# Kernel optimization log

Measured on AMD Instinct MI355X. Metric: run time of the kernel, lower is better.

Reference implementation:

```python
import jax, jax.numpy as jnp
import numpy as np

HEADS = 8
DIM_HEAD = 64
SCALE = DIM_HEAD ** -0.5


def setup_inputs() -> dict:
    key = jax.random.key(0)
    ks = jax.random.split(key, 6)
    B, T, C, H, W = 16, 64, 512, 64, 64
    inner = HEADS * DIM_HEAD  # 512
    return {
        "vision_feature": jax.random.normal(ks[0], (B, C, H, W), jnp.float32),
        "language_feature": jax.random.normal(ks[1], (B, T, C), jnp.float32),
        "mask": jnp.ones((B, T), jnp.int32),  # unused by the module's forward
        "Wq": jax.random.normal(ks[2], (inner, C), jnp.float32) * (C ** -0.5),
        "Wk": jax.random.normal(ks[3], (inner, C), jnp.float32) * (C ** -0.5),
        "Wv": jax.random.normal(ks[4], (inner, C), jnp.float32) * (C ** -0.5),
        "Wo": jax.random.normal(ks[5], (C, inner), jnp.float32) * (inner ** -0.5),
    }


def reference(vision_feature, language_feature, mask, Wq, Wk, Wv, Wo):
    B, T, C = language_feature.shape
    _, _, H, W = vision_feature.shape
    S = H * W
    # 1x1 conv projections == matmuls over the channel dim
    q = jnp.einsum('btc,ic->bti', language_feature, Wq)           # (B, T, inner)
    vis = vision_feature.reshape(B, C, S)                          # (B, C, S)
    k = jnp.einsum('ic,bcs->bis', Wk, vis)                         # (B, inner, S)
    v = jnp.einsum('ic,bcs->bis', Wv, vis)                         # (B, inner, S)
    # split heads: channel index = n*dim_head + d  (n outermost)
    q = q.reshape(B, T, HEADS, DIM_HEAD).transpose(2, 0, 1, 3)     # (h, B, T, d)
    k = k.reshape(B, HEADS, DIM_HEAD, S).transpose(1, 0, 2, 3)     # (h, B, d, S)
    v = v.reshape(B, HEADS, DIM_HEAD, S).transpose(1, 0, 3, 2)     # (h, B, S, d)
    att = jax.nn.softmax(jnp.einsum('hbtd,hbds->hbts', q, k) * SCALE, axis=-1)
    out = jnp.einsum('hbts,hbsd->hbtd', att, v)                    # (h, B, T, d)
    # merge heads back: b (n c) tokens -> equivalently (B, T, h*d)
    out = out.transpose(1, 2, 0, 3).reshape(B, T, HEADS * DIM_HEAD)
    out = jnp.einsum('bti,oi->bto', out, Wo)                       # (B, T, C)
    return out
```

## Files before the change

### kernel.cpp

```cpp
#include <hip/hip_runtime.h>
#include <stdint.h>

typedef __attribute__((ext_vector_type(8))) short short8;
typedef __attribute__((ext_vector_type(4))) short short4v;
typedef __attribute__((ext_vector_type(4))) float float4v;
typedef __attribute__((ext_vector_type(8))) __bf16 bf16x8;

#define NCH 8

__device__ __forceinline__ float4v mfma16x16x32(short8 a, short8 b, float4v c) {
  return __builtin_amdgcn_mfma_f32_16x16x32_bf16(
      __builtin_bit_cast(bf16x8, a), __builtin_bit_cast(bf16x8, b), c, 0, 0, 0);
}

__device__ __forceinline__ short f2bf(float f) {
  uint32_t u = __builtin_bit_cast(uint32_t, f);
  u += 0x7fffu + ((u >> 16) & 1u);
  return (short)(u >> 16);
}

__device__ __forceinline__ float bf2f(short s) {
  return __builtin_bit_cast(float, ((uint32_t)(uint16_t)s) << 16);
}

__device__ __forceinline__ void load_lds16(const short* g, short* l) {
  __builtin_amdgcn_global_load_lds(
      (const __attribute__((address_space(1))) void*)g,
      (__attribute__((address_space(3))) void*)l, 16, 0, 0);
}

__global__ __launch_bounds__(256) void convert5(
    const float* __restrict__ sl, short* __restrict__ dl,
    const float* __restrict__ s1, short* __restrict__ d1,
    const float* __restrict__ s2, short* __restrict__ d2,
    const float* __restrict__ s3, short* __restrict__ d3,
    const float* __restrict__ s4, short* __restrict__ d4) {
  const float* src; short* dst; int n4;
  switch (blockIdx.y) {
    case 0: src = sl; dst = dl; n4 = 131072; break;
    case 1: src = s1; dst = d1; n4 = 65536; break;
    case 2: src = s2; dst = d2; n4 = 65536; break;
    case 3: src = s3; dst = d3; n4 = 65536; break;
    default: src = s4; dst = d4; n4 = 65536; break;
  }
  const int stride = gridDim.x * blockDim.x;
  for (int i = blockIdx.x * blockDim.x + threadIdx.x; i < n4; i += stride) {
    float4v v = *(const float4v*)(src + (long)i * 4);
    short4v o;
#pragma unroll
    for (int r = 0; r < 4; r++) o[r] = f2bf(v[r]);
    *(short4v*)(dst + (long)i * 4) = o;
  }
}

template <int TRANS_STORE, int OUT_F32>
__global__ __launch_bounds__(256) void gemm_nt(
    const short* __restrict__ A, long sA,
    const short* __restrict__ B, long sB,
    void* __restrict__ C, long sC,
    int K, int ldc, float scale) {
  __shared__ alignas(16) short lA[128 * 32];
  __shared__ alignas(16) short lB[128 * 32];
  const int tid = threadIdx.x;
  const int lane = tid & 63, w = tid >> 6;
  const int quad = lane >> 4, l16 = lane & 15;
  const int wm = w >> 1, wn = w & 1;
  const long m0 = (long)blockIdx.y * 128, n0 = (long)blockIdx.x * 128;
  A += blockIdx.z * sA;
  B += blockIdx.z * sB;

  float4v acc[4][4];
#pragma unroll
  for (int i = 0; i < 4; i++)
#pragma unroll
    for (int j = 0; j < 4; j++) acc[i][j] = (float4v)0.0f;

  const int srow = tid >> 2;
  const int scol = (tid & 3) * 8;

  for (int kt = 0; kt < K; kt += 32) {
    load_lds16(&A[(m0 + srow) * K + kt + scol], &lA[tid * 8]);
    load_lds16(&A[(m0 + 64 + srow) * K + kt + scol], &lA[2048 + tid * 8]);
    load_lds16(&B[(n0 + srow) * K + kt + scol], &lB[tid * 8]);
    load_lds16(&B[(n0 + 64 + srow) * K + kt + scol], &lB[2048 + tid * 8]);
    __syncthreads();

    short8 af[4], bf[4];
#pragma unroll
    for (int t = 0; t < 4; t++) {
      af[t] = *(const short8*)&lA[(wm * 64 + t * 16 + l16) * 32 + quad * 8];
      bf[t] = *(const short8*)&lB[(wn * 64 + t * 16 + l16) * 32 + quad * 8];
    }
#pragma unroll
    for (int i = 0; i < 4; i++)
#pragma unroll
      for (int j = 0; j < 4; j++)
        acc[i][j] = mfma16x16x32(af[i], bf[j], acc[i][j]);
    __syncthreads();
  }

  const int cm = wm * 64 + quad * 4;
  const int cn = wn * 64 + l16;
  if (OUT_F32) {
    float* Cf = (float*)C + blockIdx.z * sC;
#pragma unroll
    for (int i = 0; i < 4; i++)
#pragma unroll
      for (int j = 0; j < 4; j++) {
        const long gn = n0 + cn + j * 16;
#pragma unroll
        for (int r = 0; r < 4; r++)
          Cf[(m0 + cm + i * 16 + r) * (long)ldc + gn] = acc[i][j][r] * scale;
      }
  } else if (TRANS_STORE) {
    short* Cs = (short*)C + blockIdx.z * sC;
#pragma unroll
    for (int i = 0; i < 4; i++)
#pragma unroll
      for (int j = 0; j < 4; j++) {
        const long gm = m0 + cm + i * 16;
        const long gn = n0 + cn + j * 16;
        short4v pk;
#pragma unroll
        for (int r = 0; r < 4; r++) pk[r] = f2bf(acc[i][j][r] * scale);
        *(short4v*)&Cs[gn * (long)ldc + gm] = pk;
      }
  } else {
    short* Cs = (short*)C + blockIdx.z * sC;
#pragma unroll
    for (int i = 0; i < 4; i++)
#pragma unroll
      for (int j = 0; j < 4; j++) {
        const long gn = n0 + cn + j * 16;
#pragma unroll
        for (int r = 0; r < 4; r++)
          Cs[(m0 + cm + i * 16 + r) * (long)ldc + gn] = f2bf(acc[i][j][r] * scale);
      }
  }
}

__global__ __launch_bounds__(256) void transpose_f2b(
    const float* __restrict__ vis, short* __restrict__ visT) {
  __shared__ alignas(16) short buf[64][68];
  const int tid = threadIdx.x;
  const long bz = blockIdx.z;
  const long s0 = (long)blockIdx.x * 64;
  const long c0 = (long)blockIdx.y * 64;
  const float* src = vis + bz * 512 * 4096;
  short* dst = visT + bz * 4096 * 512;
  const int tr = tid >> 4;
  const int tc4 = (tid & 15) * 4;
#pragma unroll
  for (int i = 0; i < 4; i++) {
    const int c = tr + i * 16;
    float4v val = *(const float4v*)&src[(c0 + c) * 4096 + s0 + tc4];
    buf[tc4 + 0][c] = f2bf(val[0]);
    buf[tc4 + 1][c] = f2bf(val[1]);
    buf[tc4 + 2][c] = f2bf(val[2]);
    buf[tc4 + 3][c] = f2bf(val[3]);
  }
  __syncthreads();
#pragma unroll
  for (int i = 0; i < 4; i++) {
    const int s = tr + i * 16;
    short4v val = *(const short4v*)&buf[s][tc4];
    *(short4v*)&dst[(s0 + s) * 512 + c0 + tc4] = val;
  }
}

__global__ __launch_bounds__(256) void attn_part(
    const short* __restrict__ q, const short* __restrict__ kws,
    const short* __restrict__ vws, float* __restrict__ Opart,
    float* __restrict__ lpart, int b0) {
  const int h = blockIdx.x;
  const int bz = blockIdx.y;
  const int ch = blockIdx.z;
  const int tid = threadIdx.x;
  const int lane = tid & 63, w = tid >> 6;
  const int quad = lane >> 4, l16 = lane & 15;

  __shared__ alignas(16) short lq[64 * 64];
  __shared__ alignas(16) short lk[128 * 64];
  __shared__ alignas(16) short lv[64 * 128];
  __shared__ alignas(16) short lp[64 * 128];
  __shared__ float lsum[64];

  const short* qb = q + ((long)(b0 + bz) * 64) * 512 + h * 64;
  const short* kb = kws + (long)bz * 4096 * 512 + h * 64;
  const short* vb = vws + (long)bz * 512 * 4096 + (long)h * 64 * 4096;

  if (tid < 64) lsum[tid] = 0.0f;
  load_lds16(&qb[(tid >> 3) * 512 + (tid & 7) * 8], &lq[tid * 8]);
  load_lds16(&qb[(32 + (tid >> 3)) * 512 + (tid & 7) * 8], &lq[2048 + tid * 8]);
  __syncthreads();

  short8 aq[4][2];
#pragma unroll
  for (int mt = 0; mt < 4; mt++)
#pragma unroll
    for (int ks = 0; ks < 2; ks++)
      aq[mt][ks] = *(const short8*)&lq[(mt * 16 + l16) * 64 + ks * 32 + quad * 8];

  float4v osc[4];
#pragma unroll
  for (int mt = 0; mt < 4; mt++) osc[mt] = (float4v)0.0f;
  float lrow[4][4] = {};

  const int send = ch * 512 + 512;
  for (int s0 = ch * 512; s0 < send; s0 += 128) {
#pragma unroll
    for (int it = 0; it < 4; it++) {
      const int li = tid + it * 256;
      load_lds16(&kb[(long)(s0 + (li >> 3)) * 512 + (li & 7) * 8], &lk[li * 8]);
    }
#pragma unroll
    for (int it = 0; it < 4; it++) {
      const int li = tid + it * 256;
      load_lds16(&vb[(long)(li >> 4) * 4096 + s0 + (li & 15) * 8], &lv[li * 8]);
    }
    __syncthreads();

    float4v sc[4][2];
#pragma unroll
    for (int mt = 0; mt < 4; mt++)
#pragma unroll
      for (int jn = 0; jn < 2; jn++) sc[mt][jn] = (float4v)0.0f;
#pragma unroll
    for (int ks = 0; ks < 2; ks++) {
      short8 bk[2];
#pragma unroll
      for (int jn = 0; jn < 2; jn++)
        bk[jn] = *(const short8*)&lk[((2 * w + jn) * 16 + l16) * 64 + ks * 32 + quad * 8];
#pragma unroll
      for (int mt = 0; mt < 4; mt++)
#pragma unroll
        for (int jn = 0; jn < 2; jn++)
          sc[mt][jn] = mfma16x16x32(aq[mt][ks], bk[jn], sc[mt][jn]);
    }

#pragma unroll
    for (int mt = 0; mt < 4; mt++)
#pragma unroll
      for (int jn = 0; jn < 2; jn++)
#pragma unroll
        for (int r = 0; r < 4; r++) {
          const float scv = fminf(fmaxf(sc[mt][jn][r], -80.0f), 30.0f);
          const short sp = f2bf(__expf(scv));
          lrow[mt][r] += bf2f(sp);
          lp[(mt * 16 + quad * 4 + r) * 128 + (2 * w + jn) * 16 + l16] = sp;
        }
    __syncthreads();

#pragma unroll
    for (int ks = 0; ks < 4; ks++) {
      const short8 bv = *(const short8*)&lv[(w * 16 + l16) * 128 + ks * 32 + quad * 8];
#pragma unroll
      for (int mt = 0; mt < 4; mt++) {
        const short8 ap = *(const short8*)&lp[(mt * 16 + l16) * 128 + ks * 32 + quad * 8];
        osc[mt] = mfma16x16x32(ap, bv, osc[mt]);
      }
    }
    __syncthreads();
  }

#pragma unroll
  for (int mt = 0; mt < 4; mt++)
#pragma unroll
    for (int r = 0; r < 4; r++) {
      float v = lrow[mt][r];
      v += __shfl_xor(v, 1);
      v += __shfl_xor(v, 2);
      v += __shfl_xor(v, 4);
      v += __shfl_xor(v, 8);
      if (l16 == 0) atomicAdd(&lsum[mt * 16 + quad * 4 + r], v);
    }
  __syncthreads();

  const long bh = bz * 8 + h;
  float* op = Opart + ((bh * NCH + ch) * 64) * 64 + w * 16 + l16;
#pragma unroll
  for (int mt = 0; mt < 4; mt++)
#pragma unroll
    for (int r = 0; r < 4; r++)
      op[(long)(mt * 16 + quad * 4 + r) * 64] = osc[mt][r];
  if (tid < 64) lpart[(bh * NCH + ch) * 64 + tid] = lsum[tid];
}

__global__ __launch_bounds__(256) void attn_combine(
    const float* __restrict__ Opart, const float* __restrict__ lpart,
    short* __restrict__ tmp, int b0, int nbh) {
  const int total = nbh * 4096;
  for (int idx = blockIdx.x * 256 + threadIdx.x; idx < total;
       idx += gridDim.x * 256) {
    const int bh = idx >> 12;
    const int td = idx & 4095;
    const int t = td >> 6, d = td & 63;
    float o = 0.0f, l = 0.0f;
#pragma unroll
    for (int c = 0; c < NCH; c++) {
      o += Opart[((long)bh * NCH + c) * 4096 + td];
      l += lpart[(bh * NCH + c) * 64 + t];
    }
    const int b = b0 + (bh >> 3), h = bh & 7;
    tmp[((long)b * 64 + t) * 512 + h * 64 + d] = f2bf(o / l);
  }
}

extern "C" void kernel_launch(void* const* d_in, const int* in_sizes, int n_in,
                              void* d_out, int out_size, void* d_ws, size_t ws_size,
                              hipStream_t stream) {
  (void)in_sizes; (void)n_in; (void)out_size;
  const float* vis = (const float*)d_in[0];
  const float* lang = (const float*)d_in[1];
  const float* Wq = (const float*)d_in[3];
  const float* Wk = (const float*)d_in[4];
  const float* Wv = (const float*)d_in[5];
  const float* Wo = (const float*)d_in[6];
  float* out = (float*)d_out;

  char* ws = (char*)d_ws;
  const size_t MB = 1 << 20;
  short* q_ws = (short*)(ws + 0 * MB);
  short* tmp_ws = (short*)(ws + 1 * MB);
  short* langb = (short*)(ws + 2 * MB);
  short* Wqb = (short*)(ws + 3 * MB);
  short* Wkb = (short*)(ws + 3 * MB + 512 * 1024);
  short* Wvb = (short*)(ws + 4 * MB);
  short* Wob = (short*)(ws + 4 * MB + 512 * 1024);
  char* grp = ws + 5 * MB;

  const long batch_elems = 4096l * 512;
  int g = 16;
  const int cands[5] = {1, 2, 4, 8, 16};
  for (int ci = 0; ci < 5; ci++) {
    const size_t need = 5 * MB + 3ull * (16 / cands[ci]) * batch_elems * 2;
    if (need <= ws_size) { g = cands[ci]; break; }
  }
  const int Bg = 16 / g;
  short* visT = (short*)grp;
  short* k_ws = visT + (long)Bg * batch_elems;
  short* v_ws = k_ws + (long)Bg * batch_elems;
  float* Opart = (float*)visT;
  float* lptr = Opart + (long)Bg * 262144;

  convert5<<<dim3(128, 5), 256, 0, stream>>>(lang, langb, Wq, Wqb, Wk, Wkb,
                                             Wv, Wvb, Wo, Wob);

  gemm_nt<0, 0><<<dim3(4, 8, 1), 256, 0, stream>>>(langb, 0, Wqb, 0, q_ws, 0, 512, 512, 0.125f);

  for (int gi = 0; gi < g; gi++) {
    const int b0 = gi * Bg;
    transpose_f2b<<<dim3(64, 8, Bg), 256, 0, stream>>>(vis + (long)b0 * batch_elems, visT);
    gemm_nt<1, 0><<<dim3(32, 4, Bg), 256, 0, stream>>>(Wkb, 0, visT, batch_elems, k_ws, batch_elems, 512, 512, 1.0f);
    gemm_nt<0, 0><<<dim3(32, 4, Bg), 256, 0, stream>>>(Wvb, 0, visT, batch_elems, v_ws, batch_elems, 512, 4096, 1.0f);
    attn_part<<<dim3(8, Bg, NCH), 256, 0, stream>>>(q_ws, k_ws, v_ws, Opart, lptr, b0);
    attn_combine<<<512, 256, 0, stream>>>(Opart, lptr, tmp_ws, b0, Bg * 8);
  }

  gemm_nt<0, 1><<<dim3(4, 8, 1), 256, 0, stream>>>(tmp_ws, 0, Wob, 0, out, 0, 512, 512, 1.0f);
}
```

Measured before the change: 403.7 us.

## Fuse K and V projections into one GEMM sharing vision tiles; halve attention chunks

Replaces the two separate K and V projection GEMMs with a single 512-thread kernel. Half the waves compute K and half compute V from one shared LDS tile of the transposed vision features, halving vision reads. The K output is transposed through LDS scratch so global stores are coalesced 16-byte writes instead of scattered 8-byte ones. The number of split-KV chunks in the attention kernel is reduced from 8 to 4, which cuts partial-output traffic and combine work but lowers parallelism. The combine kernel must agree with the new chunk count.

Measured after the change: 406.9 us. About the same (+0.8%).

```diff
diff --git a/kernel.cpp b/kernel.cpp
--- a/kernel.cpp
+++ b/kernel.cpp
@@ -6,7 +6,7 @@
 typedef __attribute__((ext_vector_type(4))) float float4v;
 typedef __attribute__((ext_vector_type(8))) __bf16 bf16x8;
 
-#define NCH 8
+#define NCH 4
 
 __device__ __forceinline__ float4v mfma16x16x32(short8 a, short8 b, float4v c) {
   return __builtin_amdgcn_mfma_f32_16x16x32_bf16(
@@ -53,12 +53,10 @@
   }
 }
 
-template <int TRANS_STORE, int OUT_F32>
+template <int OUT_F32>
 __global__ __launch_bounds__(256) void gemm_nt(
-    const short* __restrict__ A, long sA,
-    const short* __restrict__ B, long sB,
-    void* __restrict__ C, long sC,
-    int K, int ldc, float scale) {
+    const short* __restrict__ A, const short* __restrict__ B,
+    void* __restrict__ C, int K, int ldc, float scale) {
   __shared__ alignas(16) short lA[128 * 32];
   __shared__ alignas(16) short lB[128 * 32];
   const int tid = threadIdx.x;
@@ -66,8 +64,6 @@
   const int quad = lane >> 4, l16 = lane & 15;
   const int wm = w >> 1, wn = w & 1;
   const long m0 = (long)blockIdx.y * 128, n0 = (long)blockIdx.x * 128;
-  A += blockIdx.z * sA;
-  B += blockIdx.z * sB;
 
   float4v acc[4][4];
 #pragma unroll
@@ -102,7 +98,7 @@
   const int cm = wm * 64 + quad * 4;
   const int cn = wn * 64 + l16;
   if (OUT_F32) {
-    float* Cf = (float*)C + blockIdx.z * sC;
+    float* Cf = (float*)C;
 #pragma unroll
     for (int i = 0; i < 4; i++)
 #pragma unroll
@@ -112,21 +108,8 @@
         for (int r = 0; r < 4; r++)
           Cf[(m0 + cm + i * 16 + r) * (long)ldc + gn] = acc[i][j][r] * scale;
       }
-  } else if (TRANS_STORE) {
-    short* Cs = (short*)C + blockIdx.z * sC;
-#pragma unroll
-    for (int i = 0; i < 4; i++)
-#pragma unroll
-      for (int j = 0; j < 4; j++) {
-        const long gm = m0 + cm + i * 16;
-        const long gn = n0 + cn + j * 16;
-        short4v pk;
-#pragma unroll
-        for (int r = 0; r < 4; r++) pk[r] = f2bf(acc[i][j][r] * scale);
-        *(short4v*)&Cs[gn * (long)ldc + gm] = pk;
-      }
   } else {
-    short* Cs = (short*)C + blockIdx.z * sC;
+    short* Cs = (short*)C;
 #pragma unroll
     for (int i = 0; i < 4; i++)
 #pragma unroll
@@ -136,6 +119,99 @@
         for (int r = 0; r < 4; r++)
           Cs[(m0 + cm + i * 16 + r) * (long)ldc + gn] = f2bf(acc[i][j][r] * scale);
       }
+  }
+}
+
+__global__ __launch_bounds__(512) void gemm_kv(
+    const short* __restrict__ Wk, const short* __restrict__ Wv,
+    const short* __restrict__ visT, long sV,
+    short* __restrict__ kout, short* __restrict__ vout, long sKV) {
+  __shared__ alignas(16) short smem[12288];
+  short* lWk = smem;
+  short* lWv = smem + 4096;
+  short* lVis = smem + 8192;
+  const int tid = threadIdx.x;
+  const int lane = tid & 63, w = tid >> 6;
+  const int quad = lane >> 4, l16 = lane & 15;
+  const int role = w >> 2;
+  const int wq = w & 3, wm = wq >> 1, wn = wq & 1;
+  const long n0 = (long)blockIdx.x * 128;
+  const long m0 = (long)blockIdx.y * 128;
+  const short* vis = visT + blockIdx.z * sV;
+  short* kz = kout + blockIdx.z * sKV;
+  short* vz = vout + blockIdx.z * sKV;
+
+  float4v acc[4][4];
+#pragma unroll
+  for (int i = 0; i < 4; i++)
+#pragma unroll
+    for (int j = 0; j < 4; j++) acc[i][j] = (float4v)0.0f;
+
+  const int srow = tid >> 2;
+  const int scol = (tid & 3) * 8;
+  const short* lW = role ? lWv : lWk;
+
+  for (int kt = 0; kt < 512; kt += 32) {
+    load_lds16(&Wk[(m0 + srow) * 512 + kt + scol], &lWk[tid * 8]);
+    load_lds16(&Wv[(m0 + srow) * 512 + kt + scol], &lWv[tid * 8]);
+    load_lds16(&vis[(n0 + srow) * 512 + kt + scol], &lVis[tid * 8]);
+    __syncthreads();
+
+    short8 af[4], bf[4];
+#pragma unroll
+    for (int t = 0; t < 4; t++) {
+      af[t] = *(const short8*)&lW[(wm * 64 + t * 16 + l16) * 32 + quad * 8];
+      bf[t] = *(const short8*)&lVis[(wn * 64 + t * 16 + l16) * 32 + quad * 8];
+    }
+#pragma unroll
+    for (int i = 0; i < 4; i++)
+#pragma unroll
+      for (int j = 0; j < 4; j++)
+        acc[i][j] = mfma16x16x32(af[i], bf[j], acc[i][j]);
+    __syncthreads();
+  }
+
+  const int cm = wm * 64 + quad * 4;
+  const int cn = wn * 64 + l16;
+
+  if (role == 1) {
+#pragma unroll
+    for (int i = 0; i < 4; i++)
+#pragma unroll
+      for (int j = 0; j < 4; j++) {
+        const long gn = n0 + cn + j * 16;
+#pragma unroll
+        for (int r = 0; r < 4; r++)
+          vz[(m0 + cm + i * 16 + r) * 4096 + gn] = f2bf(acc[i][j][r]);
+      }
+  }
+
+  short* scratch = smem;
+#pragma unroll
+  for (int h = 0; h < 2; h++) {
+    __syncthreads();
+    if (role == 0 && wn == h) {
+#pragma unroll
+      for (int j = 0; j < 4; j++)
+#pragma unroll
+        for (int i = 0; i < 4; i++) {
+          const int nloc = j * 16 + l16;
+          const int m = wm * 64 + i * 16 + quad * 4;
+          short4v pk;
+#pragma unroll
+          for (int r = 0; r < 4; r++) pk[r] = f2bf(acc[i][j][r]);
+          *(short4v*)&scratch[nloc * 136 + m] = pk;
+        }
+    }
+    __syncthreads();
+    {
+      const int row = tid >> 3;
+      const int off = (tid & 7) * 16;
+      short8 v0 = *(const short8*)&scratch[row * 136 + off];
+      short8 v1 = *(const short8*)&scratch[row * 136 + off + 8];
+      *(short8*)&kz[(n0 + h * 64 + row) * 512 + m0 + off] = v0;
+      *(short8*)&kz[(n0 + h * 64 + row) * 512 + m0 + off + 8] = v1;
+    }
   }
 }
 
@@ -206,8 +282,8 @@
   for (int mt = 0; mt < 4; mt++) osc[mt] = (float4v)0.0f;
   float lrow[4][4] = {};
 
-  const int send = ch * 512 + 512;
-  for (int s0 = ch * 512; s0 < send; s0 += 128) {
+  const int send = ch * (4096 / NCH) + (4096 / NCH);
+  for (int s0 = ch * (4096 / NCH); s0 < send; s0 += 128) {
 #pragma unroll
     for (int it = 0; it < 4; it++) {
       const int li = tid + it * 256;
@@ -341,21 +417,21 @@
   short* k_ws = visT + (long)Bg * batch_elems;
   short* v_ws = k_ws + (long)Bg * batch_elems;
   float* Opart = (float*)visT;
-  float* lptr = Opart + (long)Bg * 262144;
+  float* lptr = Opart + (long)Bg * 8 * NCH * 4096;
 
   convert5<<<dim3(128, 5), 256, 0, stream>>>(lang, langb, Wq, Wqb, Wk, Wkb,
                                              Wv, Wvb, Wo, Wob);
 
-  gemm_nt<0, 0><<<dim3(4, 8, 1), 256, 0, stream>>>(langb, 0, Wqb, 0, q_ws, 0, 512, 512, 0.125f);
+  gemm_nt<0><<<dim3(4, 8), 256, 0, stream>>>(langb, Wqb, q_ws, 512, 512, 0.125f);
 
   for (int gi = 0; gi < g; gi++) {
     const int b0 = gi * Bg;
     transpose_f2b<<<dim3(64, 8, Bg), 256, 0, stream>>>(vis + (long)b0 * batch_elems, visT);
-    gemm_nt<1, 0><<<dim3(32, 4, Bg), 256, 0, stream>>>(Wkb, 0, visT, batch_elems, k_ws, batch_elems, 512, 512, 1.0f);
-    gemm_nt<0, 0><<<dim3(32, 4, Bg), 256, 0, stream>>>(Wvb, 0, visT, batch_elems, v_ws, batch_elems, 512, 4096, 1.0f);
+    gemm_kv<<<dim3(32, 4, Bg), 512, 0, stream>>>(Wkb, Wvb, visT, batch_elems,
+                                                 k_ws, v_ws, batch_elems);
     attn_part<<<dim3(8, Bg, NCH), 256, 0, stream>>>(q_ws, k_ws, v_ws, Opart, lptr, b0);
     attn_combine<<<512, 256, 0, stream>>>(Opart, lptr, tmp_ws, b0, Bg * 8);
   }
 
-  gemm_nt<0, 1><<<dim3(4, 8, 1), 256, 0, stream>>>(tmp_ws, 0, Wob, 0, out, 0, 512, 512, 1.0f);
-}
+  gemm_nt<1><<<dim3(4, 8), 256, 0, stream>>>(tmp_ws, Wob, out, 512, 512, 1.0f);
+}
```
